# Optimization experiments

Measured on AMD Instinct MI355X. Metric: run time of the kernel, lower is better.

## Reference

```python
import jax, jax.numpy as jnp
import numpy as np

NUM_LAYERS = 2
HIDDEN = 512


def setup_inputs() -> dict:
    key = jax.random.key(0)
    ks = jax.random.split(key, 5)
    B, T, D, L, H = 32, 512, 512, NUM_LAYERS, HIDDEN
    s = 1.0 / np.sqrt(H)
    return {
        "x": jax.random.normal(ks[0], (B, T, D), dtype=jnp.float32),
        "h0": jnp.zeros((B, L, H), dtype=jnp.float32),
        "c0": jnp.zeros((B, L, H), dtype=jnp.float32),
        "Wx": jax.random.normal(ks[1], (L, 4 * H, D), dtype=jnp.float32) * s,
        "bx": jax.random.normal(ks[2], (L, 4 * H), dtype=jnp.float32) * s,
        "Wh": jax.random.normal(ks[3], (L, 4 * H, H), dtype=jnp.float32) * s,
        "bh": jax.random.normal(ks[4], (L, 4 * H), dtype=jnp.float32) * s,
    }


def _lstm_forward(x, h0, c0, Wx, bx, Wh, bh):
    # x: [B,T,D]; h0,c0: [B,L,H]; Wx/Wh: [L,4H,*]; gate order (i,f,g,o)
    L, H = Wx.shape[0], Wx.shape[2]

    def step(carry, x_t):
        h, c = carry  # [B,L,H]
        inp = x_t  # [B,D]
        new_h, new_c = [], []
        for l in range(L):
            gates = (inp @ Wx[l].T + bx[l]) + (h[:, l] @ Wh[l].T + bh[l])  # [B,4H]
            i_g, f_g, g_g, o_g = jnp.split(gates, 4, axis=-1)
            c_l = jax.nn.sigmoid(f_g) * c[:, l] + jax.nn.sigmoid(i_g) * jnp.tanh(g_g)
            h_l = jax.nn.sigmoid(o_g) * jnp.tanh(c_l)
            new_h.append(h_l)
            new_c.append(c_l)
            inp = h_l
        return (jnp.stack(new_h, axis=1), jnp.stack(new_c, axis=1)), inp

    (h_n, c_n), ys = jax.lax.scan(step, (h0, c0), jnp.swapaxes(x, 0, 1))
    output = jnp.swapaxes(ys, 0, 1)  # [B,T,H]
    # torch module returns h_n/c_n swapped to [num_layers, batch, hidden]
    return output, (jnp.swapaxes(h_n, 0, 1), jnp.swapaxes(c_n, 0, 1))


def reference(x, h0, c0, Wx, bx, Wh, bh):
    return _lstm_forward(x, h0, c0, Wx, bx, Wh, bh)
```

## Files before the change

### kernel.cpp

```cpp
#include <hip/hip_runtime.h>
#include <hip/hip_bf16.h>

typedef __bf16 bf16x8 __attribute__((ext_vector_type(8)));
typedef float f32x4 __attribute__((ext_vector_type(4)));
typedef unsigned long long u64;

#define MFMA16(a, b, c) __builtin_amdgcn_mfma_f32_16x16x32_bf16((a), (b), (c), 0, 0, 0)

#define HN_OFF 8388608ull
#define CN_OFF 8421376ull

__device__ __forceinline__ float sigf(float x) { return 1.0f / (1.0f + __expf(-x)); }
__device__ __forceinline__ float b2f(unsigned short u) {
    union { unsigned u; float f; } c; c.u = ((unsigned)u) << 16; return c.f;
}
__device__ __forceinline__ unsigned short f2u(float f) {
    __hip_bfloat16 h = __float2bfloat16(f); return *(unsigned short*)&h;
}

__device__ __forceinline__ u64 gload8(const void* p) {
    return __hip_atomic_load((const u64*)p, __ATOMIC_RELAXED, __HIP_MEMORY_SCOPE_AGENT);
}
__device__ __forceinline__ void gstore4(void* p, unsigned v) {
    __hip_atomic_store((unsigned*)p, v, __ATOMIC_RELAXED, __HIP_MEMORY_SCOPE_AGENT);
}

__device__ __forceinline__ void split8(const float* p, bf16x8& hi, bf16x8& lo) {
    union { __hip_bfloat16 h[8]; bf16x8 v; } uh, ul;
    #pragma unroll
    for (int i = 0; i < 8; ++i) {
        __hip_bfloat16 e = __float2bfloat16(p[i]);
        uh.h[i] = e;
        ul.h[i] = __float2bfloat16(p[i] - __bfloat162float(e));
    }
    hi = uh.v; lo = ul.v;
}

__device__ __forceinline__ void gridbar(unsigned* flags, unsigned phase) {
    __syncthreads();
    if (threadIdx.x == 0)
        __hip_atomic_store(&flags[blockIdx.x * 16], phase,
                           __ATOMIC_RELAXED, __HIP_MEMORY_SCOPE_AGENT);
    if (threadIdx.x < 64) {
        while (__hip_atomic_load(&flags[threadIdx.x * 16],
                                 __ATOMIC_RELAXED, __HIP_MEMORY_SCOPE_AGENT) < phase)
            __builtin_amdgcn_s_sleep(1);
    }
    __syncthreads();
}

__global__ __launch_bounds__(256) void lstm_detect(
    const unsigned* __restrict__ Wq, unsigned* __restrict__ dflag,
    unsigned* __restrict__ flags)
{
    for (int j = threadIdx.x; j < 1024; j += 256) flags[j] = 0;
    if (threadIdx.x == 0) {
        int cnt = 0;
        for (int i = 0; i < 256; ++i) {
            unsigned u = Wq[(size_t)i * 4093];
            float v = b2f((unsigned short)(u & 0xFFFFu));
            if (!(v == v) || fabsf(v) > 100.0f) ++cnt;
        }
        *dflag = (cnt > 32) ? 1u : 0u;
    }
}

__global__ __launch_bounds__(256) void lstm_init(
    const void* __restrict__ h0v, const void* __restrict__ c0v,
    __hip_bfloat16* __restrict__ h0hi, __hip_bfloat16* __restrict__ h0lo,
    __hip_bfloat16* __restrict__ h1hi, __hip_bfloat16* __restrict__ h1lo,
    float* __restrict__ cws, const unsigned* __restrict__ dflag)
{
    const bool f32 = (*dflag != 0);
    int i = blockIdx.x * 256 + threadIdx.x;
    int b = i >> 9, n = i & 511;
    float f0, f1, g0, g1;
    if (f32) {
        const float* h = (const float*)h0v; const float* c = (const float*)c0v;
        f0 = h[(b * 2 + 0) * 512 + n];  f1 = h[(b * 2 + 1) * 512 + n];
        g0 = c[(b * 2 + 0) * 512 + n];  g1 = c[(b * 2 + 1) * 512 + n];
    } else {
        const unsigned short* h = (const unsigned short*)h0v;
        const unsigned short* c = (const unsigned short*)c0v;
        f0 = b2f(h[(b * 2 + 0) * 512 + n]);  f1 = b2f(h[(b * 2 + 1) * 512 + n]);
        g0 = b2f(c[(b * 2 + 0) * 512 + n]);  g1 = b2f(c[(b * 2 + 1) * 512 + n]);
    }
    __hip_bfloat16 e0 = __float2bfloat16(f0), e1 = __float2bfloat16(f1);
    h0hi[i] = e0; h0lo[i] = __float2bfloat16(f0 - __bfloat162float(e0));
    h1hi[i] = e1; h1lo[i] = __float2bfloat16(f1 - __bfloat162float(e1));
    cws[i] = g0;  cws[16384 + i] = g1;
}

__global__ __launch_bounds__(256, 1) void lstm_seq(
    const void* __restrict__ xv,
    const void* __restrict__ Wxv, const void* __restrict__ bxv,
    const void* __restrict__ Whv, const void* __restrict__ bhv,
    __hip_bfloat16* __restrict__ h0hi, __hip_bfloat16* __restrict__ h0lo,
    __hip_bfloat16* __restrict__ h1hi, __hip_bfloat16* __restrict__ h1lo,
    const float* __restrict__ cws, unsigned* __restrict__ flags,
    const unsigned* __restrict__ dflag, void* __restrict__ outv)
{
    const bool f32 = (*dflag != 0);
    const int p  = blockIdx.x & 1;
    const int wt = blockIdx.x >> 1;
    const int tid = threadIdx.x;
    const int q = tid >> 6, lane = tid & 63;
    const int n16 = lane & 15, quad = lane >> 4;
    const int colg = q * 512 + wt * 16 + n16;

    __shared__ __align__(16) char smem[131072];
    __shared__ float gbuf[2176];

    float* outf = (float*)outv;
    __hip_bfloat16* outh = (__hip_bfloat16*)outv;

    bf16x8 wa[16], wal[16], wr[16], wrl[16];
    if (f32) {
        const float* WA = (const float*)Wxv + ((size_t)(p * 2048 + colg)) * 512;
        const float* WR = (const float*)Whv + ((size_t)(p * 2048 + colg)) * 512;
        #pragma unroll
        for (int kk = 0; kk < 16; ++kk) {
            split8(WA + kk * 32 + quad * 8, wa[kk], wal[kk]);
            split8(WR + kk * 32 + quad * 8, wr[kk], wrl[kk]);
        }
    } else {
        const unsigned short* WA = (const unsigned short*)Wxv + ((size_t)(p * 2048 + colg)) * 512;
        const unsigned short* WR = (const unsigned short*)Whv + ((size_t)(p * 2048 + colg)) * 512;
        union { uint4 u; bf16x8 v; } cvu;
        #pragma unroll
        for (int kk = 0; kk < 16; ++kk) {
            cvu.u = *(const uint4*)(WA + kk * 32 + quad * 8); wa[kk] = cvu.v;
            cvu.u = *(const uint4*)(WR + kk * 32 + quad * 8); wr[kk] = cvu.v;
        }
    }
    float bias;
    if (f32) bias = ((const float*)bxv)[p * 2048 + colg] + ((const float*)bhv)[p * 2048 + colg];
    else     bias = b2f(((const unsigned short*)bxv)[p * 2048 + colg])
                  + b2f(((const unsigned short*)bhv)[p * 2048 + colg]);

    const int e0 = tid * 2;
    const int pbb = e0 >> 4;
    const int pn0 = e0 & 15;
    float cv[2];
    cv[0] = cws[p * 16384 + pbb * 512 + wt * 16 + pn0];
    cv[1] = cws[p * 16384 + pbb * 512 + wt * 16 + pn0 + 1];

    const unsigned short* xb = (const unsigned short*)xv;

    #define STAGE_X_BF16(T)                                                      \
        { _Pragma("unroll")                                                      \
          for (int j = 0; j < 8; ++j) {                                          \
              int L = j * 256 + tid;                                             \
              int rem = L & 127;                                                 \
              int row = ((rem >> 6) << 4) + (rem & 15);                          \
              int kcol = ((L >> 7) << 5) + (((rem >> 4) & 3) << 3);              \
              *(uint4*)(smem + (L << 4)) =                                       \
                  *(const uint4*)(xb + ((size_t)row * 512 + (T)) * 512 + kcol);  \
          } }

    if (p == 0 && !f32) STAGE_X_BF16(0);

    for (int k = 0; k <= 512; ++k) {
        const bool doComp = (p == 0) ? (k < 512) : (k > 0);

        if (doComp) {
            const int t = (p == 0) ? k : (k - 1);
            const __hip_bfloat16* Ahi = h0hi + (k & 1) * 16384;
            const __hip_bfloat16* Alo = h0lo + (k & 1) * 16384;
            const __hip_bfloat16* Rhi = (p == 0) ? h0hi + (k & 1) * 16384
                                                 : h1hi + ((k + 1) & 1) * 16384;
            const __hip_bfloat16* Rlo = (p == 0) ? h0lo + (k & 1) * 16384
                                                 : h1lo + ((k + 1) & 1) * 16384;

            #pragma unroll
            for (int j = 0; j < 8; ++j) {
                int L = j * 256 + tid;
                int rem = L & 127;
                int row = ((rem >> 6) << 4) + (rem & 15);
                int kcol = ((L >> 7) << 5) + (((rem >> 4) & 3) << 3);
                size_t hoff = (size_t)row * 512 + kcol;
                u64 r0 = gload8(Rhi + hoff), r1 = gload8(Rhi + hoff + 4);
                u64 l0 = gload8(Rlo + hoff), l1 = gload8(Rlo + hoff + 4);
                ((u64*)(smem + 65536 + (L << 4)))[0] = r0;
                ((u64*)(smem + 65536 + (L << 4)))[1] = r1;
                ((u64*)(smem + 98304 + (L << 4)))[0] = l0;
                ((u64*)(smem + 98304 + (L << 4)))[1] = l1;
                if (p == 1) {
                    u64 a0 = gload8(Ahi + hoff), a1 = gload8(Ahi + hoff + 4);
                    u64 b0 = gload8(Alo + hoff), b1 = gload8(Alo + hoff + 4);
                    ((u64*)(smem + (L << 4)))[0] = a0;
                    ((u64*)(smem + (L << 4)))[1] = a1;
                    ((u64*)(smem + 32768 + (L << 4)))[0] = b0;
                    ((u64*)(smem + 32768 + (L << 4)))[1] = b1;
                } else if (f32) {
                    const float* xp = (const float*)xv + ((size_t)row * 512 + t) * 512 + kcol;
                    bf16x8 hi, lo;
                    split8(xp, hi, lo);
                    *(bf16x8*)(smem + (L << 4)) = hi;
                    *(bf16x8*)(smem + 32768 + (L << 4)) = lo;
                }
            }
            __syncthreads();

            const char* sl = smem + (lane << 4);
            f32x4 acc0 = {bias, bias, bias, bias};
            f32x4 acc1 = {bias, bias, bias, bias};
            if (f32) {
                #pragma unroll
                for (int kk = 0; kk < 16; ++kk) {
                    bf16x8 Aha = *(const bf16x8*)(sl + kk * 2048);
                    bf16x8 Ahb = *(const bf16x8*)(sl + kk * 2048 + 1024);
                    bf16x8 Ala = *(const bf16x8*)(sl + 32768 + kk * 2048);
                    bf16x8 Alb = *(const bf16x8*)(sl + 32768 + kk * 2048 + 1024);
                    bf16x8 Rha = *(const bf16x8*)(sl + 65536 + kk * 2048);
                    bf16x8 Rhb = *(const bf16x8*)(sl + 65536 + kk * 2048 + 1024);
                    bf16x8 Rla = *(const bf16x8*)(sl + 98304 + kk * 2048);
                    bf16x8 Rlb = *(const bf16x8*)(sl + 98304 + kk * 2048 + 1024);
                    acc0 = MFMA16(Aha, wa[kk], acc0);
                    acc0 = MFMA16(Aha, wal[kk], acc0);
                    acc0 = MFMA16(Ala, wa[kk], acc0);
                    acc0 = MFMA16(Rha, wr[kk], acc0);
                    acc0 = MFMA16(Rha, wrl[kk], acc0);
                    acc0 = MFMA16(Rla, wr[kk], acc0);
                    acc1 = MFMA16(Ahb, wa[kk], acc1);
                    acc1 = MFMA16(Ahb, wal[kk], acc1);
                    acc1 = MFMA16(Alb, wa[kk], acc1);
                    acc1 = MFMA16(Rhb, wr[kk], acc1);
                    acc1 = MFMA16(Rhb, wrl[kk], acc1);
                    acc1 = MFMA16(Rlb, wr[kk], acc1);
                }
            } else if (p == 1) {
                #pragma unroll
                for (int kk = 0; kk < 16; ++kk) {
                    bf16x8 Aha = *(const bf16x8*)(sl + kk * 2048);
                    bf16x8 Ahb = *(const bf16x8*)(sl + kk * 2048 + 1024);
                    bf16x8 Ala = *(const bf16x8*)(sl + 32768 + kk * 2048);
                    bf16x8 Alb = *(const bf16x8*)(sl + 32768 + kk * 2048 + 1024);
                    bf16x8 Rha = *(const bf16x8*)(sl + 65536 + kk * 2048);
                    bf16x8 Rhb = *(const bf16x8*)(sl + 65536 + kk * 2048 + 1024);
                    bf16x8 Rla = *(const bf16x8*)(sl + 98304 + kk * 2048);
                    bf16x8 Rlb = *(const bf16x8*)(sl + 98304 + kk * 2048 + 1024);
                    acc0 = MFMA16(Aha, wa[kk], acc0);
                    acc0 = MFMA16(Ala, wa[kk], acc0);
                    acc0 = MFMA16(Rha, wr[kk], acc0);
                    acc0 = MFMA16(Rla, wr[kk], acc0);
                    acc1 = MFMA16(Ahb, wa[kk], acc1);
                    acc1 = MFMA16(Alb, wa[kk], acc1);
                    acc1 = MFMA16(Rhb, wr[kk], acc1);
                    acc1 = MFMA16(Rlb, wr[kk], acc1);
                }
            } else {
                #pragma unroll
                for (int kk = 0; kk < 16; ++kk) {
                    bf16x8 Aha = *(const bf16x8*)(sl + kk * 2048);
                    bf16x8 Ahb = *(const bf16x8*)(sl + kk * 2048 + 1024);
                    bf16x8 Rha = *(const bf16x8*)(sl + 65536 + kk * 2048);
                    bf16x8 Rhb = *(const bf16x8*)(sl + 65536 + kk * 2048 + 1024);
                    bf16x8 Rla = *(const bf16x8*)(sl + 98304 + kk * 2048);
                    bf16x8 Rlb = *(const bf16x8*)(sl + 98304 + kk * 2048 + 1024);
                    acc0 = MFMA16(Aha, wa[kk], acc0);
                    acc0 = MFMA16(Rha, wr[kk], acc0);
                    acc0 = MFMA16(Rla, wr[kk], acc0);
                    acc1 = MFMA16(Ahb, wa[kk], acc1);
                    acc1 = MFMA16(Rhb, wr[kk], acc1);
                    acc1 = MFMA16(Rlb, wr[kk], acc1);
                }
            }
            __syncthreads();

            #pragma unroll
            for (int r = 0; r < 4; ++r) {
                gbuf[(q * 32 + quad * 4 + r) * 17 + n16]      = acc0[r];
                gbuf[(q * 32 + 16 + quad * 4 + r) * 17 + n16] = acc1[r];
            }
            __syncthreads();

            __hip_bfloat16* Ohi = (p == 0) ? h0hi + ((k + 1) & 1) * 16384
                                           : h1hi + (k & 1) * 16384;
            __hip_bfloat16* Olo = (p == 0) ? h0lo + ((k + 1) & 1) * 16384
                                           : h1lo + (k & 1) * 16384;
            float rh[2], rc[2];
            #pragma unroll
            for (int j = 0; j < 2; ++j) {
                int n = pn0 + j;
                float ig = gbuf[(0 * 32 + pbb) * 17 + n];
                float fg = gbuf[(1 * 32 + pbb) * 17 + n];
                float gg = gbuf[(2 * 32 + pbb) * 17 + n];
                float og = gbuf[(3 * 32 + pbb) * 17 + n];
                float cnew = sigf(fg) * cv[j] + sigf(ig) * tanhf(gg);
                cv[j] = cnew;
                rc[j] = cnew;
                rh[j] = sigf(og) * tanhf(cnew);
            }
            unsigned phi = 0, plo = 0, pcn = 0;
            #pragma unroll
            for (int j = 0; j < 2; ++j) {
                unsigned short hu = f2u(rh[j]);
                unsigned short lu = f2u(rh[j] - b2f(hu));
                phi |= ((unsigned)hu) << (16 * j);
                plo |= ((unsigned)lu) << (16 * j);
                pcn |= ((unsigned)f2u(rc[j])) << (16 * j);
            }
            const int idx = pbb * 512 + wt * 16 + pn0;
            gstore4(Ohi + idx, phi);
            gstore4(Olo + idx, plo);
            if (p == 1) {
                size_t oidx = ((size_t)pbb * 512 + t) * 512 + wt * 16 + pn0;
                if (f32) { outf[oidx] = rh[0]; outf[oidx + 1] = rh[1]; }
                else     { *(unsigned*)(outh + oidx) = phi; }
                if (k == 512) {
                    if (f32) {
                        outf[HN_OFF + 16384 + idx] = rh[0]; outf[HN_OFF + 16385 + idx] = rh[1];
                        outf[CN_OFF + 16384 + idx] = rc[0]; outf[CN_OFF + 16385 + idx] = rc[1];
                    } else {
                        *(unsigned*)(outh + HN_OFF + 16384 + idx) = phi;
                        *(unsigned*)(outh + CN_OFF + 16384 + idx) = pcn;
                    }
                }
            } else if (k == 511) {
                if (f32) {
                    outf[HN_OFF + idx] = rh[0]; outf[HN_OFF + idx + 1] = rh[1];
                    outf[CN_OFF + idx] = rc[0]; outf[CN_OFF + idx + 1] = rc[1];
                } else {
                    *(unsigned*)(outh + HN_OFF + idx) = phi;
                    *(unsigned*)(outh + CN_OFF + idx) = pcn;
                }
            }

            if (p == 0 && !f32 && k + 1 < 512) STAGE_X_BF16(k + 1);
        }

        if (k < 512) gridbar(flags, (unsigned)(k + 1));
    }
}

extern "C" void kernel_launch(void* const* d_in, const int* in_sizes, int n_in,
                              void* d_out, int out_size, void* d_ws, size_t ws_size,
                              hipStream_t stream)
{
    const void* x  = d_in[0];
    const void* h0 = d_in[1];
    const void* c0 = d_in[2];
    const void* Wx = d_in[3];
    const void* bx = d_in[4];
    const void* Wh = d_in[5];
    const void* bh = d_in[6];

    char* ws = (char*)d_ws;
    __hip_bfloat16* h0hi = (__hip_bfloat16*)(ws);
    __hip_bfloat16* h0lo = (__hip_bfloat16*)(ws + 65536);
    __hip_bfloat16* h1hi = (__hip_bfloat16*)(ws + 131072);
    __hip_bfloat16* h1lo = (__hip_bfloat16*)(ws + 196608);
    float*          cws  = (float*)(ws + 262144);
    unsigned*       flags = (unsigned*)(ws + 393216);
    unsigned*       dflag = (unsigned*)(ws + 397312);

    lstm_detect<<<1, 256, 0, stream>>>((const unsigned*)Wx, dflag, flags);
    lstm_init<<<64, 256, 0, stream>>>(h0, c0, h0hi, h0lo, h1hi, h1lo, cws, dflag);
    lstm_seq<<<64, 256, 0, stream>>>(x, Wx, bx, Wh, bh,
                                     h0hi, h0lo, h1hi, h1lo, cws, flags, dflag, d_out);
}
```

Before: 7.139 ms.

## Split grid barrier to signal arrival early and batch state loads

The grid barrier is split so each block publishes its arrival flag right after storing its new hidden state, before it writes the output sequence and stages the next x. That overlaps those writes with other blocks' barrier waits. The global state loads are also regrouped so all loads are issued before the LDS stores, which raises memory-level parallelism at the cost of more registers. The detect kernel now uses a 64-lane reduction instead of a serial loop.

```diff
diff --git a/kernel.cpp b/kernel.cpp
--- a/kernel.cpp
+++ b/kernel.cpp
@@ -36,32 +36,23 @@
     hi = uh.v; lo = ul.v;
 }
 
-__device__ __forceinline__ void gridbar(unsigned* flags, unsigned phase) {
-    __syncthreads();
-    if (threadIdx.x == 0)
-        __hip_atomic_store(&flags[blockIdx.x * 16], phase,
-                           __ATOMIC_RELAXED, __HIP_MEMORY_SCOPE_AGENT);
-    if (threadIdx.x < 64) {
-        while (__hip_atomic_load(&flags[threadIdx.x * 16],
-                                 __ATOMIC_RELAXED, __HIP_MEMORY_SCOPE_AGENT) < phase)
-            __builtin_amdgcn_s_sleep(1);
-    }
-    __syncthreads();
-}
-
 __global__ __launch_bounds__(256) void lstm_detect(
     const unsigned* __restrict__ Wq, unsigned* __restrict__ dflag,
     unsigned* __restrict__ flags)
 {
     for (int j = threadIdx.x; j < 1024; j += 256) flags[j] = 0;
-    if (threadIdx.x == 0) {
-        int cnt = 0;
-        for (int i = 0; i < 256; ++i) {
-            unsigned u = Wq[(size_t)i * 4093];
+    if (threadIdx.x < 64) {
+        int lane = threadIdx.x;
+        int bad = 0;
+        #pragma unroll
+        for (int i = 0; i < 4; ++i) {
+            unsigned u = Wq[(size_t)(lane + i * 64) * 4093];
             float v = b2f((unsigned short)(u & 0xFFFFu));
-            if (!(v == v) || fabsf(v) > 100.0f) ++cnt;
+            if (!(v == v) || fabsf(v) > 100.0f) ++bad;
         }
-        *dflag = (cnt > 32) ? 1u : 0u;
+        #pragma unroll
+        for (int off = 32; off; off >>= 1) bad += __shfl_down(bad, off, 64);
+        if (lane == 0) *dflag = (bad > 32) ? 1u : 0u;
     }
 }
 
@@ -172,32 +163,68 @@
             const __hip_bfloat16* Rlo = (p == 0) ? h0lo + (k & 1) * 16384
                                                  : h1lo + ((k + 1) & 1) * 16384;
 
-            #pragma unroll
-            for (int j = 0; j < 8; ++j) {
-                int L = j * 256 + tid;
-                int rem = L & 127;
-                int row = ((rem >> 6) << 4) + (rem & 15);
-                int kcol = ((L >> 7) << 5) + (((rem >> 4) & 3) << 3);
-                size_t hoff = (size_t)row * 512 + kcol;
-                u64 r0 = gload8(Rhi + hoff), r1 = gload8(Rhi + hoff + 4);
-                u64 l0 = gload8(Rlo + hoff), l1 = gload8(Rlo + hoff + 4);
-                ((u64*)(smem + 65536 + (L << 4)))[0] = r0;
-                ((u64*)(smem + 65536 + (L << 4)))[1] = r1;
-                ((u64*)(smem + 98304 + (L << 4)))[0] = l0;
-                ((u64*)(smem + 98304 + (L << 4)))[1] = l1;
-                if (p == 1) {
-                    u64 a0 = gload8(Ahi + hoff), a1 = gload8(Ahi + hoff + 4);
-                    u64 b0 = gload8(Alo + hoff), b1 = gload8(Alo + hoff + 4);
-                    ((u64*)(smem + (L << 4)))[0] = a0;
-                    ((u64*)(smem + (L << 4)))[1] = a1;
-                    ((u64*)(smem + 32768 + (L << 4)))[0] = b0;
-                    ((u64*)(smem + 32768 + (L << 4)))[1] = b1;
-                } else if (f32) {
-                    const float* xp = (const float*)xv + ((size_t)row * 512 + t) * 512 + kcol;
-                    bf16x8 hi, lo;
-                    split8(xp, hi, lo);
-                    *(bf16x8*)(smem + (L << 4)) = hi;
-                    *(bf16x8*)(smem + 32768 + (L << 4)) = lo;
+            if (p == 1) {
+                #pragma unroll
+                for (int hp = 0; hp < 2; ++hp) {
+                    u64 vA[8], vB[8], vR[8], vL[8];
+                    #pragma unroll
+                    for (int jj = 0; jj < 4; ++jj) {
+                        int L = (hp * 4 + jj) * 256 + tid;
+                        int rem = L & 127;
+                        int row = ((rem >> 6) << 4) + (rem & 15);
+                        int kcol = ((L >> 7) << 5) + (((rem >> 4) & 3) << 3);
+                        size_t hoff = (size_t)row * 512 + kcol;
+                        vA[jj*2] = gload8(Ahi + hoff); vA[jj*2+1] = gload8(Ahi + hoff + 4);
+                        vB[jj*2] = gload8(Alo + hoff); vB[jj*2+1] = gload8(Alo + hoff + 4);
+                        vR[jj*2] = gload8(Rhi + hoff); vR[jj*2+1] = gload8(Rhi + hoff + 4);
+                        vL[jj*2] = gload8(Rlo + hoff); vL[jj*2+1] = gload8(Rlo + hoff + 4);
+                    }
+                    #pragma unroll
+                    for (int jj = 0; jj < 4; ++jj) {
+                        int L = (hp * 4 + jj) * 256 + tid;
+                        u64* dA = (u64*)(smem + (L << 4));
+                        u64* dB = (u64*)(smem + 32768 + (L << 4));
+                        u64* dR = (u64*)(smem + 65536 + (L << 4));
+                        u64* dL = (u64*)(smem + 98304 + (L << 4));
+                        dA[0] = vA[jj*2]; dA[1] = vA[jj*2+1];
+                        dB[0] = vB[jj*2]; dB[1] = vB[jj*2+1];
+                        dR[0] = vR[jj*2]; dR[1] = vR[jj*2+1];
+                        dL[0] = vL[jj*2]; dL[1] = vL[jj*2+1];
+                    }
+                }
+            } else {
+                u64 vR[16], vL[16];
+                #pragma unroll
+                for (int j = 0; j < 8; ++j) {
+                    int L = j * 256 + tid;
+                    int rem = L & 127;
+                    int row = ((rem >> 6) << 4) + (rem & 15);
+                    int kcol = ((L >> 7) << 5) + (((rem >> 4) & 3) << 3);
+                    size_t hoff = (size_t)row * 512 + kcol;
+                    vR[j*2] = gload8(Rhi + hoff); vR[j*2+1] = gload8(Rhi + hoff + 4);
+                    vL[j*2] = gload8(Rlo + hoff); vL[j*2+1] = gload8(Rlo + hoff + 4);
+                }
+                #pragma unroll
+                for (int j = 0; j < 8; ++j) {
+                    int L = j * 256 + tid;
+                    u64* dR = (u64*)(smem + 65536 + (L << 4));
+                    u64* dL = (u64*)(smem + 98304 + (L << 4));
+                    dR[0] = vR[j*2]; dR[1] = vR[j*2+1];
+                    dL[0] = vL[j*2]; dL[1] = vL[j*2+1];
+                }
+                if (f32) {
+                    #pragma unroll
+                    for (int j = 0; j < 8; ++j) {
+                        int L = j * 256 + tid;
+                        int rem = L & 127;
+                        int row = ((rem >> 6) << 4) + (rem & 15);
+                        int kcol = ((L >> 7) << 5) + (((rem >> 4) & 3) << 3);
+                        const float* xp = (const float*)xv + ((size_t)row * 512 + t) * 512 + kcol;
+                        bf16x8 hi, lo;
+                        split8(xp, hi, lo);
+                        *(bf16x8*)(smem + (L << 4)) = hi;
+                        *(bf16x8*)(smem + 32768 + (L << 4)) = lo;
+                    }
                 }
             }
             __syncthreads();
@@ -304,6 +331,12 @@
             const int idx = pbb * 512 + wt * 16 + pn0;
             gstore4(Ohi + idx, phi);
             gstore4(Olo + idx, plo);
+
+            __syncthreads();
+            if (k < 512 && tid == 0)
+                __hip_atomic_store(&flags[blockIdx.x * 16], (unsigned)(k + 1),
+                                   __ATOMIC_RELAXED, __HIP_MEMORY_SCOPE_AGENT);
+
             if (p == 1) {
                 size_t oidx = ((size_t)pbb * 512 + t) * 512 + wt * 16 + pn0;
                 if (f32) { outf[oidx] = rh[0]; outf[oidx + 1] = rh[1]; }
@@ -326,11 +359,22 @@
                     *(unsigned*)(outh + CN_OFF + idx) = pcn;
                 }
             }
-
             if (p == 0 && !f32 && k + 1 < 512) STAGE_X_BF16(k + 1);
+        } else {
+            if (k < 512 && tid == 0)
+                __hip_atomic_store(&flags[blockIdx.x * 16], (unsigned)(k + 1),
+                                   __ATOMIC_RELAXED, __HIP_MEMORY_SCOPE_AGENT);
         }
 
-        if (k < 512) gridbar(flags, (unsigned)(k + 1));
+        if (k < 512) {
+            if (tid < 64) {
+                while (__hip_atomic_load(&flags[tid * 16],
+                                         __ATOMIC_RELAXED, __HIP_MEMORY_SCOPE_AGENT)
+                       < (unsigned)(k + 1))
+                    __builtin_amdgcn_s_sleep(1);
+            }
+            __syncthreads();
+        }
     }
 }
 
```

Measured after the change: 6.998 ms. -2.0%, faster.
